# Optimization experiments

Hardware: AMD Instinct MI355X
Metric: run time of the kernel (lower is better)

## Reference

```python
import jax, jax.numpy as jnp
import numpy as np

N, E, FS = 50000, 400000, 256
H, D = 8, 64            # GAT heads, hidden_size (per-head out_feats)
NH, DK, DV = 8, 64, 64  # transformer MHA
B = 1024
NEG_SLOPE = 0.2
EPS = 1e-6


def _layer_norm(x, g, b, eps=EPS):
    mu = x.mean(-1, keepdims=True)
    var = x.var(-1, keepdims=True)
    return (x - mu) / jnp.sqrt(var + eps) * g + b


def setup_inputs() -> dict:
    key = jax.random.key(0)
    ks = jax.random.split(key, 20)
    s = 0.02
    return {
        "features": jax.random.normal(ks[0], (N, FS), jnp.float32),
        "src": jax.random.randint(ks[1], (E,), 0, N, jnp.int32),
        "dst": jax.random.randint(ks[2], (E,), 0, N, jnp.int32),
        "url": jax.random.randint(ks[3], (B,), 1, N + 1, jnp.int32),  # 1-based ids
        # GATConv params (DGL-style)
        "gat_fc_w": jax.random.normal(ks[4], (FS, H * D), jnp.float32) * s,
        "attn_l": jax.random.normal(ks[5], (H, D), jnp.float32) * s,
        "attn_r": jax.random.normal(ks[6], (H, D), jnp.float32) * s,
        "gat_res_w": jax.random.normal(ks[7], (FS, H * D), jnp.float32) * s,
        "gat_bias": jnp.zeros((H, D), jnp.float32),
        # post-GAT LayerNorm
        "ln_g": jnp.ones((D,), jnp.float32),
        "ln_b": jnp.zeros((D,), jnp.float32),
        # MultiHeadAttention params
        "wq": jax.random.normal(ks[8], (D, NH * DK), jnp.float32) * s,
        "wk": jax.random.normal(ks[9], (D, NH * DK), jnp.float32) * s,
        "wv": jax.random.normal(ks[10], (D, NH * DV), jnp.float32) * s,
        "fc_w": jax.random.normal(ks[11], (NH * DV, D), jnp.float32) * s,
        "fc_b": jnp.zeros((D,), jnp.float32),
        "mha_ln_g": jnp.ones((D,), jnp.float32),
        "mha_ln_b": jnp.zeros((D,), jnp.float32),
        # final classifier
        "out_w": jax.random.normal(ks[12], (D, 2), jnp.float32) * s,
        "out_b": jnp.zeros((2,), jnp.float32),
    }


def reference(features, src, dst, url, gat_fc_w, attn_l, attn_r, gat_res_w,
              gat_bias, ln_g, ln_b, wq, wk, wv, fc_w, fc_b, mha_ln_g,
              mha_ln_b, out_w, out_b):
    # ---- GATConv (residual=True, bias, negative_slope=0.2, no activation) ----
    feat = (features @ gat_fc_w).reshape(N, H, D)          # [N,H,D]
    el = jnp.einsum('nhd,hd->nh', feat, attn_l)            # [N,H]
    er = jnp.einsum('nhd,hd->nh', feat, attn_r)            # [N,H]
    e = jax.nn.leaky_relu(el[src] + er[dst], NEG_SLOPE)    # [E,H] edge scores
    # segment softmax over incoming edges of each dst node
    m = jax.ops.segment_max(e, dst, num_segments=N)        # [N,H]
    m = jnp.where(jnp.isfinite(m), m, 0.0)
    ex = jnp.exp(e - m[dst])                               # [E,H]
    denom = jax.ops.segment_sum(ex, dst, num_segments=N)   # [N,H]
    a = ex / jnp.maximum(denom[dst], 1e-20)                # [E,H]
    msg = feat[src] * a[:, :, None]                        # [E,H,D]
    rst = jax.ops.segment_sum(msg, dst, num_segments=N)    # [N,H,D]
    res = (features @ gat_res_w).reshape(N, H, D)
    gat_emb = rst + res + gat_bias                         # [N,H,D]

    # ---- select batch nodes (url is 1-based) ----
    ids = url - 1
    x = gat_emb[ids]                                       # [B,H,D]
    x = _layer_norm(x, ln_g, ln_b)

    # ---- dense multi-head self-attention over the H gat heads (seq dim) ----
    residual = x
    q = (x @ wq).reshape(B, H, NH, DK)
    k = (x @ wk).reshape(B, H, NH, DK)
    v = (x @ wv).reshape(B, H, NH, DV)
    attn = jnp.einsum('bqhd,bkhd->bhqk', q, k) / jnp.sqrt(jnp.float32(DK))
    attn = jax.nn.softmax(attn, axis=-1)
    o = jnp.einsum('bhqk,bkhd->bqhd', attn, v).reshape(B, H, NH * DV)
    o = o @ fc_w + fc_b                                    # [B,H,D]
    o = _layer_norm(o + residual, mha_ln_g, mha_ln_b)

    # ---- pool + classify ----
    pooled = o.sum(axis=1)                                 # [B,D]
    logits = pooled @ out_w + out_b                        # [B,2]
    return logits
```

## Files before the change

### kernel.cpp

```cpp
#include <hip/hip_runtime.h>
#include <math.h>

#define Nn 50000
#define Ee 400000
#define FSz 256
#define HD_ 512
#define Bb 1024

static __device__ __forceinline__ int clampi(int v, int lo, int hi){
    return v < lo ? lo : (v > hi ? hi : v);
}
static __device__ __forceinline__ unsigned short f2bf(float f){
    unsigned int u = __float_as_uint(f);
    unsigned int r = u + 0x7FFFu + ((u >> 16) & 1u);
    return (unsigned short)(r >> 16);
}
static __device__ __forceinline__ float bflo(unsigned int v){ return __uint_as_float(v << 16); }
static __device__ __forceinline__ float bfhi(unsigned int v){ return __uint_as_float(v & 0xFFFF0000u); }

__global__ __launch_bounds__(256) void k_mark(const int* __restrict__ url, int* uid, int* unode, int* cnt,
                                              const float* __restrict__ W,
                                              const float* __restrict__ al,
                                              const float* __restrict__ ar,
                                              float* __restrict__ wl, float* __restrict__ wr){
    int t = threadIdx.x;
    if(blockIdx.x == 4){
        __shared__ float sal[512], sar[512];
        sal[t] = al[t]; sal[t+256] = al[t+256];
        sar[t] = ar[t]; sar[t+256] = ar[t+256];
        __syncthreads();
        const float4* Wr = (const float4*)(W + t*512);
        float accl[8] = {0,0,0,0,0,0,0,0};
        float accr[8] = {0,0,0,0,0,0,0,0};
        for(int i = 0; i < 128; i++){
            float4 w = Wr[i];
            int o = 4*i;
            int h = o >> 6;
            const float* alp = &sal[o];
            const float* arp = &sar[o];
            accl[h] += w.x*alp[0] + w.y*alp[1] + w.z*alp[2] + w.w*alp[3];
            accr[h] += w.x*arp[0] + w.y*arp[1] + w.z*arp[2] + w.w*arp[3];
        }
        #pragma unroll
        for(int h = 0; h < 8; h++){ wl[h*256 + t] = accl[h]; wr[h*256 + t] = accr[h]; }
    } else {
        int b = blockIdx.x * 256 + t;
        if(b < Bb){
            int n = clampi(url[b] - 1, 0, Nn - 1);
            int old = atomicCAS(&uid[n], -1, -2);
            if(old == -1){
                int id = atomicAdd(cnt, 1);
                unode[id] = n;
                uid[n] = id;
            }
        }
    }
}

__global__ __launch_bounds__(256) void k_scatter(const int* __restrict__ src, const int* __restrict__ dst,
                                                 const int* __restrict__ uid, int* __restrict__ fill,
                                                 int* __restrict__ slist){
    int e = blockIdx.x * 256 + threadIdx.x;
    if(e >= Ee) return;
    int d = dst[e];
    if((unsigned)d >= (unsigned)Nn) return;
    int u = uid[d];
    if(u < 0) return;
    int pos = atomicAdd(&fill[u], 1);
    if(pos >= 64) return;
    slist[u*64 + pos] = clampi(src[e], 0, Nn - 1);
}

__global__ __launch_bounds__(256) void k_gat(const float* __restrict__ features,
                                             const float* __restrict__ Wfc,
                                             const float* __restrict__ Wres,
                                             const float* __restrict__ bias,
                                             const float* __restrict__ wl,
                                             const float* __restrict__ wr,
                                             const int* __restrict__ cnt, const int* __restrict__ unode,
                                             const int* __restrict__ fill, const int* __restrict__ slist,
                                             float* __restrict__ gemb){
    int t = threadIdx.x;
    int lane = t & 63, wv = t >> 6;
    int cntv = cnt[0];
    int u0 = blockIdx.x * 2;
    if(u0 >= cntv) return;

    __shared__ float cxs[2][8][256];
    __shared__ float fres[2][256];
    __shared__ float sew[2][64][8];
    __shared__ float ser[2][8];
    __shared__ int   sslist[2][64];

    float4 rwl[8], rwr[8];
    #pragma unroll
    for(int h = 0; h < 8; h++){
        rwl[h] = *(const float4*)&wl[h*256 + 4*lane];
        rwr[h] = *(const float4*)&wr[h*256 + 4*lane];
    }

    int dg[2];
    dg[0] = min(fill[u0], 64);
    dg[1] = (u0 + 1 < cntv) ? min(fill[u0 + 1], 64) : 0;
    #pragma unroll
    for(int j = 0; j < 2; j++){
        int u = u0 + j;
        if(t < dg[j]) sslist[j][t] = slist[u*64 + t];
        if(u < cntv) fres[j][t] = features[(size_t)unode[u] * FSz + t];
        else         fres[j][t] = 0.f;
    }
    __syncthreads();

    int total = dg[0] + dg[1];
    for(int tau = wv; tau < total + 2; tau += 4){
        int j, i, s, isEr;
        if(tau < dg[0]){ j = 0; i = tau; s = sslist[0][i]; isEr = 0; }
        else if(tau < total){ j = 1; i = tau - dg[0]; s = sslist[1][i]; isEr = 0; }
        else { j = tau - total; i = 0; s = (u0 + j < cntv) ? unode[u0 + j] : 0; isEr = 1; }
        float4 x = *(const float4*)(features + (size_t)s * FSz + 4*lane);
        float p[8];
        if(isEr){
            #pragma unroll
            for(int h = 0; h < 8; h++)
                p[h] = x.x*rwr[h].x + x.y*rwr[h].y + x.z*rwr[h].z + x.w*rwr[h].w;
        } else {
            #pragma unroll
            for(int h = 0; h < 8; h++)
                p[h] = x.x*rwl[h].x + x.y*rwl[h].y + x.z*rwl[h].z + x.w*rwl[h].w;
        }
        #pragma unroll
        for(int h = 0; h < 8; h++){
            #pragma unroll
            for(int m = 32; m >= 1; m >>= 1) p[h] += __shfl_xor(p[h], m, 64);
        }
        if(lane == 0){
            if(isEr){
                #pragma unroll
                for(int h = 0; h < 8; h++) ser[j][h] = p[h];
            } else {
                #pragma unroll
                for(int h = 0; h < 8; h++) sew[j][i][h] = p[h];
            }
        }
    }
    __syncthreads();
    if(t < 16){
        int j = t >> 3, h = t & 7;
        int dgj = dg[j];
        if(dgj > 0){
            float ern = ser[j][h];
            float m = -1e30f;
            for(int i = 0; i < dgj; i++){
                float v = sew[j][i][h] + ern;
                v = v > 0.f ? v : 0.2f * v;
                m = fmaxf(m, v);
            }
            float sum = 0.f;
            for(int i = 0; i < dgj; i++){
                float v = sew[j][i][h] + ern;
                v = v > 0.f ? v : 0.2f * v;
                float w = expf(v - m);
                sum += w;
                sew[j][i][h] = w;
            }
            float inv = 1.0f / fmaxf(sum, 1e-20f);
            for(int i = 0; i < dgj; i++) sew[j][i][h] *= inv;
        }
    }
    __syncthreads();
    #pragma unroll
    for(int j = 0; j < 2; j++){
        float cx[8] = {0,0,0,0,0,0,0,0};
        for(int i = 0; i < dg[j]; i++){
            int s = sslist[j][i];
            float x = features[(size_t)s * FSz + t];
            const float* av = &sew[j][i][0];
            #pragma unroll
            for(int h = 0; h < 8; h++) cx[h] += av[h] * x;
        }
        #pragma unroll
        for(int h = 0; h < 8; h++) cxs[j][h][t] = cx[h];
    }
    __syncthreads();

    int h = t >> 5;
    int o0 = 2 * t;
    const float2* Wfc2  = (const float2*)Wfc;
    const float2* Wres2 = (const float2*)Wres;
    float a00 = 0.f, a01 = 0.f, a10 = 0.f, a11 = 0.f;
    for(int f = 0; f < 256; f += 4){
        float2 w0 = Wfc2[(f+0)*256 + t];
        float2 w1 = Wfc2[(f+1)*256 + t];
        float2 w2 = Wfc2[(f+2)*256 + t];
        float2 w3 = Wfc2[(f+3)*256 + t];
        float2 r0 = Wres2[(f+0)*256 + t];
        float2 r1 = Wres2[(f+1)*256 + t];
        float2 r2 = Wres2[(f+2)*256 + t];
        float2 r3 = Wres2[(f+3)*256 + t];
        float4 c0 = *(const float4*)&cxs[0][h][f];
        float4 x0 = *(const float4*)&fres[0][f];
        float4 c1 = *(const float4*)&cxs[1][h][f];
        float4 x1 = *(const float4*)&fres[1][f];
        a00 += c0.x*w0.x + c0.y*w1.x + c0.z*w2.x + c0.w*w3.x + x0.x*r0.x + x0.y*r1.x + x0.z*r2.x + x0.w*r3.x;
        a01 += c0.x*w0.y + c0.y*w1.y + c0.z*w2.y + c0.w*w3.y + x0.x*r0.y + x0.y*r1.y + x0.z*r2.y + x0.w*r3.y;
        a10 += c1.x*w0.x + c1.y*w1.x + c1.z*w2.x + c1.w*w3.x + x1.x*r0.x + x1.y*r1.x + x1.z*r2.x + x1.w*r3.x;
        a11 += c1.x*w0.y + c1.y*w1.y + c1.z*w2.y + c1.w*w3.y + x1.x*r0.y + x1.y*r1.y + x1.z*r2.y + x1.w*r3.y;
    }
    float b0 = bias[o0], b1 = bias[o0 + 1];
    {
        float2* gp = (float2*)(gemb + (size_t)u0 * HD_);
        gp[t] = make_float2(a00 + b0, a01 + b1);
    }
    if(u0 + 1 < cntv){
        float2* gp = (float2*)(gemb + (size_t)(u0 + 1) * HD_);
        gp[t] = make_float2(a10 + b0, a11 + b1);
    }
}

__global__ __launch_bounds__(256, 4) void k_mha(const int* __restrict__ url, const int* __restrict__ uid,
                                             const float* __restrict__ gemb,
                                             const float* __restrict__ lng, const float* __restrict__ lnb,
                                             const float* __restrict__ wq, const float* __restrict__ wk,
                                             const float* __restrict__ wvp, const float* __restrict__ fcw,
                                             const float* __restrict__ fcb, const float* __restrict__ mlg,
                                             const float* __restrict__ mlb, const float* __restrict__ outw,
                                             const float* __restrict__ outb, float* __restrict__ out){
    __shared__ float A[512];
    __shared__ float xnF[512];
    __shared__ unsigned short xnT[64*8];
    __shared__ unsigned short qkb[2*8*520];
    __shared__ float mu8[8], rs8[8], pooled[64];

    int b = blockIdx.x, t = threadIdx.x;
    int lane = t & 63, wv = t >> 6;
    int n = clampi(url[b] - 1, 0, Nn - 1);
    int u = uid[n];
    if(u < 0) u = 0;
    const float* gp = gemb + (size_t)u * HD_;
    A[t] = gp[t]; A[t + 256] = gp[t + 256];
    __syncthreads();
    if(t < 8){
        float s = 0.f, s2 = 0.f;
        for(int d = 0; d < 64; d++){ float v = A[t*64 + d]; s += v; s2 += v * v; }
        float mu = s * (1.0f/64.0f);
        float var = s2 * (1.0f/64.0f) - mu * mu;
        mu8[t] = mu; rs8[t] = rsqrtf(fmaxf(var, 0.0f) + 1e-6f);
    }
    __syncthreads();
    #pragma unroll
    for(int p = 0; p < 2; p++){
        int i = p*256 + t; int q = i >> 6, d = i & 63;
        float xv = (A[i] - mu8[q]) * rs8[q] * lng[d] + lnb[d];
        xnF[i] = xv;
        xnT[d*8 + q] = f2bf(xv);
    }
    __syncthreads();
    float aq0[8] = {0,0,0,0,0,0,0,0}, aq1[8] = {0,0,0,0,0,0,0,0};
    float ak0[8] = {0,0,0,0,0,0,0,0}, ak1[8] = {0,0,0,0,0,0,0,0};
    float av0[8] = {0,0,0,0,0,0,0,0}, av1[8] = {0,0,0,0,0,0,0,0};
    #pragma unroll 2
    for(int d = 0; d < 64; d++){
        float q0 = wq[d*512 + t],  q1 = wq[d*512 + t + 256];
        float k0 = wk[d*512 + t],  k1 = wk[d*512 + t + 256];
        float v0 = wvp[d*512 + t], v1 = wvp[d*512 + t + 256];
        uint4 xp = *(const uint4*)&xnT[d*8];
        float xv[8] = { bflo(xp.x), bfhi(xp.x), bflo(xp.y), bfhi(xp.y),
                        bflo(xp.z), bfhi(xp.z), bflo(xp.w), bfhi(xp.w) };
        #pragma unroll
        for(int r = 0; r < 8; r++){
            aq0[r] += xv[r]*q0; aq1[r] += xv[r]*q1;
            ak0[r] += xv[r]*k0; ak1[r] += xv[r]*k1;
            av0[r] += xv[r]*v0; av1[r] += xv[r]*v1;
        }
    }
    #pragma unroll
    for(int qq = 0; qq < 8; qq++){
        qkb[qq*520 + t]              = f2bf(aq0[qq]);
        qkb[qq*520 + t + 256]        = f2bf(aq1[qq]);
        qkb[4160 + qq*520 + t]       = f2bf(ak0[qq]);
        qkb[4160 + qq*520 + t + 256] = f2bf(ak1[qq]);
    }
    __syncthreads();
    #pragma unroll
    for(int p = 0; p < 2; p++){
        int idx = p*256 + t;
        int nh = idx >> 6, qq = (idx >> 3) & 7, kk = idx & 7;
        const unsigned short* qrow = &qkb[qq*520 + nh*64];
        const unsigned short* krow = &qkb[4160 + kk*520 + nh*64];
        float s = 0.f;
        #pragma unroll
        for(int d8 = 0; d8 < 64; d8 += 8){
            uint4 qv = *(const uint4*)&qrow[d8];
            uint4 kv = *(const uint4*)&krow[d8];
            s += bflo(qv.x)*bflo(kv.x) + bfhi(qv.x)*bfhi(kv.x)
               + bflo(qv.y)*bflo(kv.y) + bfhi(qv.y)*bfhi(kv.y)
               + bflo(qv.z)*bflo(kv.z) + bfhi(qv.z)*bfhi(kv.z)
               + bflo(qv.w)*bflo(kv.w) + bfhi(qv.w)*bfhi(kv.w);
        }
        A[idx] = s * 0.125f;
    }
    __syncthreads();
    if(t < 64){
        float mx = -1e30f;
        #pragma unroll
        for(int k = 0; k < 8; k++) mx = fmaxf(mx, A[t*8 + k]);
        float e[8]; float s = 0.f;
        #pragma unroll
        for(int k = 0; k < 8; k++){ e[k] = expf(A[t*8 + k] - mx); s += e[k]; }
        float inv = 1.0f / s;
        #pragma unroll
        for(int k = 0; k < 8; k++) A[t*8 + k] = e[k] * inv;
    }
    __syncthreads();
    {
        int nh0 = wv;
        #pragma unroll
        for(int qq = 0; qq < 8; qq++){
            const float* s0 = &A[nh0*64 + qq*8];
            const float* s1 = &A[(nh0+4)*64 + qq*8];
            float4 a0 = *(const float4*)s0, b0 = *(const float4*)(s0 + 4);
            float4 a1 = *(const float4*)s1, b1 = *(const float4*)(s1 + 4);
            float o0 = a0.x*av0[0] + a0.y*av0[1] + a0.z*av0[2] + a0.w*av0[3]
                     + b0.x*av0[4] + b0.y*av0[5] + b0.z*av0[6] + b0.w*av0[7];
            float o1 = a1.x*av1[0] + a1.y*av1[1] + a1.z*av1[2] + a1.w*av1[3]
                     + b1.x*av1[4] + b1.y*av1[5] + b1.z*av1[6] + b1.w*av1[7];
            qkb[qq*520 + t]       = f2bf(o0);
            qkb[qq*520 + t + 256] = f2bf(o1);
        }
    }
    __syncthreads();
    {
        float* P = (float*)&qkb[4160];
        int g = lane & 31;
        int qh = lane >> 5;
        int k0 = wv * 128;
        float a[4][2] = {{0,0},{0,0},{0,0},{0,0}};
        const float2* fw2 = (const float2*)fcw;
        for(int k = k0; k < k0 + 128; k += 8){
            float2 f0 = fw2[(k+0)*32 + g];
            float2 f1 = fw2[(k+1)*32 + g];
            float2 f2 = fw2[(k+2)*32 + g];
            float2 f3 = fw2[(k+3)*32 + g];
            float2 f4 = fw2[(k+4)*32 + g];
            float2 f5 = fw2[(k+5)*32 + g];
            float2 f6 = fw2[(k+6)*32 + g];
            float2 f7 = fw2[(k+7)*32 + g];
            #pragma unroll
            for(int jq = 0; jq < 4; jq++){
                int qq = qh*4 + jq;
                uint4 op = *(const uint4*)&qkb[qq*520 + k];
                float x0 = bflo(op.x), x1 = bfhi(op.x), x2 = bflo(op.y), x3 = bfhi(op.y);
                float x4 = bflo(op.z), x5 = bfhi(op.z), x6 = bflo(op.w), x7 = bfhi(op.w);
                a[jq][0] += x0*f0.x + x1*f1.x + x2*f2.x + x3*f3.x + x4*f4.x + x5*f5.x + x6*f6.x + x7*f7.x;
                a[jq][1] += x0*f0.y + x1*f1.y + x2*f2.y + x3*f3.y + x4*f4.y + x5*f5.y + x6*f6.y + x7*f7.y;
            }
        }
        __syncthreads();
        #pragma unroll
        for(int jq = 0; jq < 4; jq++){
            int qq = qh*4 + jq;
            *(float2*)&P[wv*512 + qq*64 + 2*g] = make_float2(a[jq][0], a[jq][1]);
        }
        __syncthreads();
        #pragma unroll
        for(int p = 0; p < 2; p++){
            int o = p*256 + t;
            int dd = o & 63;
            A[o] = P[o] + P[512 + o] + P[1024 + o] + P[1536 + o] + fcb[dd] + xnF[o];
        }
    }
    __syncthreads();
    if(t < 8){
        float s = 0.f, s2 = 0.f;
        for(int d = 0; d < 64; d++){ float v = A[t*64 + d]; s += v; s2 += v * v; }
        float mu = s * (1.0f/64.0f);
        float var = s2 * (1.0f/64.0f) - mu * mu;
        mu8[t] = mu; rs8[t] = rsqrtf(fmaxf(var, 0.0f) + 1e-6f);
    }
    __syncthreads();
    if(t < 64){
        float g2 = mlg[t], bb = mlb[t];
        float s = 0.f;
        #pragma unroll
        for(int qq = 0; qq < 8; qq++)
            s += (A[qq*64 + t] - mu8[qq]) * rs8[qq] * g2 + bb;
        pooled[t] = s;
    }
    __syncthreads();
    if(t < 2){
        float s = outb[t];
        for(int d = 0; d < 64; d++) s += pooled[d] * outw[d*2 + t];
        out[b*2 + t] = s;
    }
}

extern "C" void kernel_launch(void* const* d_in, const int* in_sizes, int n_in,
                              void* d_out, int out_size, void* d_ws, size_t ws_size,
                              hipStream_t stream){
    (void)in_sizes; (void)n_in; (void)out_size; (void)ws_size;
    const float* features  = (const float*)d_in[0];
    const int*   src       = (const int*)d_in[1];
    const int*   dst       = (const int*)d_in[2];
    const int*   url       = (const int*)d_in[3];
    const float* gat_fc_w  = (const float*)d_in[4];
    const float* attn_l    = (const float*)d_in[5];
    const float* attn_r    = (const float*)d_in[6];
    const float* gat_res_w = (const float*)d_in[7];
    const float* gat_bias  = (const float*)d_in[8];
    const float* ln_g      = (const float*)d_in[9];
    const float* ln_b      = (const float*)d_in[10];
    const float* wq        = (const float*)d_in[11];
    const float* wk        = (const float*)d_in[12];
    const float* wv        = (const float*)d_in[13];
    const float* fc_w      = (const float*)d_in[14];
    const float* fc_b      = (const float*)d_in[15];
    const float* mha_ln_g  = (const float*)d_in[16];
    const float* mha_ln_b  = (const float*)d_in[17];
    const float* out_w     = (const float*)d_in[18];
    const float* out_b     = (const float*)d_in[19];

    char* base = (char*)d_ws;
    size_t cur = 0;
    auto alloc = [&](size_t nbytes) -> void* {
        void* p = base + cur;
        cur = (cur + nbytes + 255) & ~(size_t)255;
        return p;
    };
    float* wl    = (float*)alloc(2048 * sizeof(float));
    float* wr    = (float*)alloc(2048 * sizeof(float));
    int*   uid   = (int*)alloc((size_t)Nn * sizeof(int));
    int*   unode = (int*)alloc(1024 * sizeof(int));
    int*   fill  = (int*)alloc(1056 * sizeof(int));
    int*   cnt   = fill + 1024;
    int*   slist = (int*)alloc((size_t)1024 * 64 * sizeof(int));
    float* gemb  = (float*)alloc((size_t)1024 * 512 * sizeof(float));

    hipMemsetAsync(uid, 0xFF, (size_t)Nn * sizeof(int), stream);
    hipMemsetAsync(fill, 0, 1056 * sizeof(int), stream);

    hipLaunchKernelGGL(k_mark,    dim3(5),    dim3(256), 0, stream, url, uid, unode, cnt,
                       gat_fc_w, attn_l, attn_r, wl, wr);
    hipLaunchKernelGGL(k_scatter, dim3(1563), dim3(256), 0, stream, src, dst, uid, fill, slist);
    hipLaunchKernelGGL(k_gat,     dim3(512),  dim3(256), 0, stream, features, gat_fc_w, gat_res_w, gat_bias,
                       wl, wr, cnt, unode, fill, slist, gemb);
    hipLaunchKernelGGL(k_mha,     dim3(1024), dim3(256), 0, stream, url, uid, gemb, ln_g, ln_b,
                       wq, wk, wv, fc_w, fc_b, mha_ln_g, mha_ln_b, out_w, out_b,
                       (float*)d_out);
}
```

Before: 238.2 us.

## Process four batch nodes per GAT block and parallelize attention-weight folding

The GAT kernel now handles four unique batch nodes per block instead of two. Each Wfc/Wres weight load is reused across four rows, which halves the total weight traffic from global memory, and neighbor feature gathers for the four nodes are interleaved. The wl/wr fold of attn vectors into the fc weights is spread over 16 blocks using wave-wide shuffle reductions instead of one block with per-thread serial loops. The cost is more shared memory and registers per GAT block and only 256 blocks, which lowers occupancy and adds imbalance when node degrees differ.

```diff
diff --git a/kernel.cpp b/kernel.cpp
--- a/kernel.cpp
+++ b/kernel.cpp
@@ -24,25 +24,32 @@
                                               const float* __restrict__ ar,
                                               float* __restrict__ wl, float* __restrict__ wr){
     int t = threadIdx.x;
-    if(blockIdx.x == 4){
-        __shared__ float sal[512], sar[512];
-        sal[t] = al[t]; sal[t+256] = al[t+256];
-        sar[t] = ar[t]; sar[t+256] = ar[t+256];
-        __syncthreads();
-        const float4* Wr = (const float4*)(W + t*512);
-        float accl[8] = {0,0,0,0,0,0,0,0};
-        float accr[8] = {0,0,0,0,0,0,0,0};
-        for(int i = 0; i < 128; i++){
-            float4 w = Wr[i];
-            int o = 4*i;
-            int h = o >> 6;
-            const float* alp = &sal[o];
-            const float* arp = &sar[o];
-            accl[h] += w.x*alp[0] + w.y*alp[1] + w.z*alp[2] + w.w*alp[3];
-            accr[h] += w.x*arp[0] + w.y*arp[1] + w.z*arp[2] + w.w*arp[3];
-        }
-        #pragma unroll
-        for(int h = 0; h < 8; h++){ wl[h*256 + t] = accl[h]; wr[h*256 + t] = accr[h]; }
+    if(blockIdx.x >= 4){
+        int bi = blockIdx.x - 4;
+        int wv = t >> 6, lane = t & 63;
+        #pragma unroll
+        for(int r = 0; r < 4; r++){
+            int f = bi*16 + wv*4 + r;
+            float pl[8], pr[8];
+            #pragma unroll
+            for(int h = 0; h < 8; h++){
+                float w = W[f*512 + h*64 + lane];
+                pl[h] = w * al[h*64 + lane];
+                pr[h] = w * ar[h*64 + lane];
+            }
+            #pragma unroll
+            for(int h = 0; h < 8; h++){
+                #pragma unroll
+                for(int m = 32; m >= 1; m >>= 1){
+                    pl[h] += __shfl_xor(pl[h], m, 64);
+                    pr[h] += __shfl_xor(pr[h], m, 64);
+                }
+            }
+            #pragma unroll
+            for(int h = 0; h < 8; h++){
+                if(lane == h){ wl[h*256 + f] = pl[h]; wr[h*256 + f] = pr[h]; }
+            }
+        }
     } else {
         int b = blockIdx.x * 256 + t;
         if(b < Bb){
@@ -83,14 +90,16 @@
     int t = threadIdx.x;
     int lane = t & 63, wv = t >> 6;
     int cntv = cnt[0];
-    int u0 = blockIdx.x * 2;
+    int u0 = blockIdx.x * 4;
     if(u0 >= cntv) return;
 
-    __shared__ float cxs[2][8][256];
-    __shared__ float fres[2][256];
-    __shared__ float sew[2][64][8];
-    __shared__ float ser[2][8];
-    __shared__ int   sslist[2][64];
+    __shared__ float cxs[4][8][256];
+    __shared__ float fres[4][256];
+    __shared__ float sew[4][64][8];
+    __shared__ float ser[4][8];
+    __shared__ int   sslist[4][64];
+
+    for(int i = t; i < 4*64*8; i += 256) ((float*)sew)[i] = 0.f;
 
     float4 rwl[8], rwr[8];
     #pragma unroll
@@ -99,24 +108,27 @@
         rwr[h] = *(const float4*)&wr[h*256 + 4*lane];
     }
 
-    int dg[2];
-    dg[0] = min(fill[u0], 64);
-    dg[1] = (u0 + 1 < cntv) ? min(fill[u0 + 1], 64) : 0;
-    #pragma unroll
-    for(int j = 0; j < 2; j++){
+    int dg[4];
+    #pragma unroll
+    for(int j = 0; j < 4; j++){
         int u = u0 + j;
+        dg[j] = (u < cntv) ? min(fill[u], 64) : 0;
         if(t < dg[j]) sslist[j][t] = slist[u*64 + t];
         if(u < cntv) fres[j][t] = features[(size_t)unode[u] * FSz + t];
         else         fres[j][t] = 0.f;
     }
     __syncthreads();
 
-    int total = dg[0] + dg[1];
-    for(int tau = wv; tau < total + 2; tau += 4){
-        int j, i, s, isEr;
-        if(tau < dg[0]){ j = 0; i = tau; s = sslist[0][i]; isEr = 0; }
-        else if(tau < total){ j = 1; i = tau - dg[0]; s = sslist[1][i]; isEr = 0; }
-        else { j = tau - total; i = 0; s = (u0 + j < cntv) ? unode[u0 + j] : 0; isEr = 1; }
+    int c1 = dg[0], c2 = c1 + dg[1], c3 = c2 + dg[2];
+    int total = c3 + dg[3];
+    for(int tau = wv; tau < total + 4; tau += 4){
+        int j, i, isEr = 0;
+        if(tau < c1){ j = 0; i = tau; }
+        else if(tau < c2){ j = 1; i = tau - c1; }
+        else if(tau < c3){ j = 2; i = tau - c2; }
+        else if(tau < total){ j = 3; i = tau - c3; }
+        else { j = tau - total; i = 0; isEr = 1; }
+        int s = isEr ? ((u0 + j < cntv) ? unode[u0 + j] : 0) : sslist[j][i];
         float4 x = *(const float4*)(features + (size_t)s * FSz + 4*lane);
         float p[8];
         if(isEr){
@@ -144,7 +156,7 @@
         }
     }
     __syncthreads();
-    if(t < 16){
+    if(t < 32){
         int j = t >> 3, h = t & 7;
         int dgj = dg[j];
         if(dgj > 0){
@@ -168,18 +180,32 @@
         }
     }
     __syncthreads();
-    #pragma unroll
-    for(int j = 0; j < 2; j++){
-        float cx[8] = {0,0,0,0,0,0,0,0};
-        for(int i = 0; i < dg[j]; i++){
-            int s = sslist[j][i];
-            float x = features[(size_t)s * FSz + t];
-            const float* av = &sew[j][i][0];
-            #pragma unroll
-            for(int h = 0; h < 8; h++) cx[h] += av[h] * x;
-        }
-        #pragma unroll
-        for(int h = 0; h < 8; h++) cxs[j][h][t] = cx[h];
+    {
+        float cx[4][8];
+        #pragma unroll
+        for(int j = 0; j < 4; j++)
+            #pragma unroll
+            for(int h = 0; h < 8; h++) cx[j][h] = 0.f;
+        int mxd = max(max(dg[0], dg[1]), max(dg[2], dg[3]));
+        for(int i = 0; i < mxd; i++){
+            float x[4];
+            #pragma unroll
+            for(int j = 0; j < 4; j++){
+                int s = (i < dg[j]) ? sslist[j][i] : 0;
+                x[j] = features[(size_t)s * FSz + t];
+            }
+            #pragma unroll
+            for(int j = 0; j < 4; j++){
+                const float* av = &sew[j][i][0];
+                float xm = (i < dg[j]) ? x[j] : 0.f;
+                #pragma unroll
+                for(int h = 0; h < 8; h++) cx[j][h] += av[h] * xm;
+            }
+        }
+        #pragma unroll
+        for(int j = 0; j < 4; j++)
+            #pragma unroll
+            for(int h = 0; h < 8; h++) cxs[j][h][t] = cx[j][h];
     }
     __syncthreads();
 
@@ -187,7 +213,7 @@
     int o0 = 2 * t;
     const float2* Wfc2  = (const float2*)Wfc;
     const float2* Wres2 = (const float2*)Wres;
-    float a00 = 0.f, a01 = 0.f, a10 = 0.f, a11 = 0.f;
+    float a[4][2] = {{0,0},{0,0},{0,0},{0,0}};
     for(int f = 0; f < 256; f += 4){
         float2 w0 = Wfc2[(f+0)*256 + t];
         float2 w1 = Wfc2[(f+1)*256 + t];
@@ -197,23 +223,23 @@
         float2 r1 = Wres2[(f+1)*256 + t];
         float2 r2 = Wres2[(f+2)*256 + t];
         float2 r3 = Wres2[(f+3)*256 + t];
-        float4 c0 = *(const float4*)&cxs[0][h][f];
-        float4 x0 = *(const float4*)&fres[0][f];
-        float4 c1 = *(const float4*)&cxs[1][h][f];
-        float4 x1 = *(const float4*)&fres[1][f];
-        a00 += c0.x*w0.x + c0.y*w1.x + c0.z*w2.x + c0.w*w3.x + x0.x*r0.x + x0.y*r1.x + x0.z*r2.x + x0.w*r3.x;
-        a01 += c0.x*w0.y + c0.y*w1.y + c0.z*w2.y + c0.w*w3.y + x0.x*r0.y + x0.y*r1.y + x0.z*r2.y + x0.w*r3.y;
-        a10 += c1.x*w0.x + c1.y*w1.x + c1.z*w2.x + c1.w*w3.x + x1.x*r0.x + x1.y*r1.x + x1.z*r2.x + x1.w*r3.x;
-        a11 += c1.x*w0.y + c1.y*w1.y + c1.z*w2.y + c1.w*w3.y + x1.x*r0.y + x1.y*r1.y + x1.z*r2.y + x1.w*r3.y;
+        #pragma unroll
+        for(int j = 0; j < 4; j++){
+            float4 c = *(const float4*)&cxs[j][h][f];
+            float4 x = *(const float4*)&fres[j][f];
+            a[j][0] += c.x*w0.x + c.y*w1.x + c.z*w2.x + c.w*w3.x
+                     + x.x*r0.x + x.y*r1.x + x.z*r2.x + x.w*r3.x;
+            a[j][1] += c.x*w0.y + c.y*w1.y + c.z*w2.y + c.w*w3.y
+                     + x.x*r0.y + x.y*r1.y + x.z*r2.y + x.w*r3.y;
+        }
     }
     float b0 = bias[o0], b1 = bias[o0 + 1];
-    {
-        float2* gp = (float2*)(gemb + (size_t)u0 * HD_);
-        gp[t] = make_float2(a00 + b0, a01 + b1);
-    }
-    if(u0 + 1 < cntv){
-        float2* gp = (float2*)(gemb + (size_t)(u0 + 1) * HD_);
-        gp[t] = make_float2(a10 + b0, a11 + b1);
+    #pragma unroll
+    for(int j = 0; j < 4; j++){
+        if(u0 + j < cntv){
+            float2* gp = (float2*)(gemb + (size_t)(u0 + j) * HD_);
+            gp[t] = make_float2(a[j][0] + b0, a[j][1] + b1);
+        }
     }
 }
 
@@ -438,10 +464,10 @@
     hipMemsetAsync(uid, 0xFF, (size_t)Nn * sizeof(int), stream);
     hipMemsetAsync(fill, 0, 1056 * sizeof(int), stream);
 
-    hipLaunchKernelGGL(k_mark,    dim3(5),    dim3(256), 0, stream, url, uid, unode, cnt,
+    hipLaunchKernelGGL(k_mark,    dim3(20),   dim3(256), 0, stream, url, uid, unode, cnt,
                        gat_fc_w, attn_l, attn_r, wl, wr);
     hipLaunchKernelGGL(k_scatter, dim3(1563), dim3(256), 0, stream, src, dst, uid, fill, slist);
-    hipLaunchKernelGGL(k_gat,     dim3(512),  dim3(256), 0, stream, features, gat_fc_w, gat_res_w, gat_bias,
+    hipLaunchKernelGGL(k_gat,     dim3(256),  dim3(256), 0, stream, features, gat_fc_w, gat_res_w, gat_bias,
                        wl, wr, cnt, unode, fill, slist, gemb);
     hipLaunchKernelGGL(k_mha,     dim3(1024), dim3(256), 0, stream, url, uid, gemb, ln_g, ln_b,
                        wq, wk, wv, fc_w, fc_b, mha_ln_g, mha_ln_b, out_w, out_b,
```

Result: faster. 220.9 us (-7.3%).
